# Kernel tuning notes

Measured on AMD Instinct MI355X. Metric: run time of the kernel, lower is better.

## Reference

```python
import jax, jax.numpy as jnp
import numpy as np

TOP_K = 4
N_GROUP = 4
TOPK_GROUP = 2
ROUTED_SCALING = 1.0


def setup_inputs() -> dict:
    key = jax.random.key(0)
    k1, k2, k3, k4, k5 = jax.random.split(key, 5)
    B, S, H, I, E = 1, 2048, 1024, 512, 16
    hidden_states = jax.random.normal(k1, (B, S, H), dtype=jnp.float32)
    # router weight (kaiming-uniform-like scale)
    gate_weight = jax.random.normal(k2, (E, H), dtype=jnp.float32) * (1.0 / np.sqrt(H))
    e_bias = jnp.zeros((E,), dtype=jnp.float32)  # e_score_correction_bias buffer
    gate_proj = jax.random.normal(k3, (E, I, H), dtype=jnp.float32) * 0.02
    up_proj = jax.random.normal(k4, (E, I, H), dtype=jnp.float32) * 0.02
    down_proj = jax.random.normal(k5, (E, H, I), dtype=jnp.float32) * 0.02
    return {
        "hidden_states": hidden_states,
        "gate_weight": gate_weight,
        "e_bias": e_bias,
        "gate_proj": gate_proj,
        "up_proj": up_proj,
        "down_proj": down_proj,
    }


def _route(x_flat, gate_weight, e_bias):
    # x_flat: [T, H]
    T = x_flat.shape[0]
    E = gate_weight.shape[0]
    logits = jnp.einsum("th,eh->te", x_flat, gate_weight)
    scores = jax.nn.sigmoid(logits)                      # [T, E]
    scores_for_choice = scores + e_bias[None, :]
    # group scores = sum of top-2 expert scores within each group
    grp = scores_for_choice.reshape(T, N_GROUP, E // N_GROUP)
    top2, _ = jax.lax.top_k(grp, 2)
    group_scores = top2.sum(axis=-1)                     # [T, G]
    _, group_idx = jax.lax.top_k(group_scores, TOPK_GROUP)
    group_mask = jax.nn.one_hot(group_idx, N_GROUP, dtype=scores.dtype).sum(axis=1)  # [T, G]
    score_mask = jnp.repeat(group_mask, E // N_GROUP, axis=1)                        # [T, E]
    tmp_scores = jnp.where(score_mask > 0, scores_for_choice, 0.0)
    _, topk_idx = jax.lax.top_k(tmp_scores, TOP_K)       # [T, K]
    topk_weight = jnp.take_along_axis(scores, topk_idx, axis=1)
    denom = topk_weight.sum(axis=-1, keepdims=True) + 1e-20
    topk_weight = topk_weight / denom * ROUTED_SCALING
    return topk_idx, topk_weight


def reference(hidden_states, gate_weight, e_bias, gate_proj, up_proj, down_proj):
    B, S, H = hidden_states.shape
    E = gate_proj.shape[0]
    x = hidden_states.reshape(-1, H).astype(jnp.float32)  # [T, H]
    topk_idx, topk_weight = _route(x, gate_weight, e_bias)
    # combine weights per (token, expert): sum over the k slots selecting e
    combine = (jax.nn.one_hot(topk_idx, E, dtype=x.dtype) * topk_weight[..., None]).sum(axis=1)  # [T, E]
    # dense expert MLP (mathematically equal to gather-compute-scatter since
    # non-selected experts receive zero combine weight)
    g = jnp.einsum("th,eih->tei", x, gate_proj)
    u = jnp.einsum("th,eih->tei", x, up_proj)
    act = jax.nn.silu(g) * u                              # [T, E, I]
    expert_out = jnp.einsum("tei,ehi->teh", act, down_proj)
    y = jnp.einsum("teh,te->th", expert_out, combine)
    return y.reshape(B, S, H)
```

## Files before the change

kernel.cpp:

```cpp
#include <hip/hip_runtime.h>
#include <hip/hip_bf16.h>

typedef __attribute__((ext_vector_type(8))) short bf16x8;
typedef __attribute__((ext_vector_type(4))) float f32x4;

#define T_TOK 2048
#define HD 1024
#define ID 512
#define NE 16
#define TOPK 4
#define BK 32
#define WELEM (HD*ID*NE)
#define CPAD 16

__device__ __forceinline__ unsigned pk2(float a, float b) {
    return __builtin_amdgcn_perm(__float_as_uint(b), __float_as_uint(a),
                                 0x07060302u);
}
__device__ __forceinline__ bf16x8 cvt8(const float* __restrict__ p) {
    float4 a = *(const float4*)p;
    float4 b = *(const float4*)(p + 4);
    union { bf16x8 v; unsigned u[4]; } r;
    r.u[0] = pk2(a.x, a.y); r.u[1] = pk2(a.z, a.w);
    r.u[2] = pk2(b.x, b.y); r.u[3] = pk2(b.z, b.w);
    return r.v;
}
__device__ __forceinline__ short f2bf(float f) {
    unsigned u = __float_as_uint(f);
    return (short)((u + 0x7fffu + ((u >> 16) & 1u)) >> 16);
}
__device__ __forceinline__ float bf2f(short s) {
    return __uint_as_float(((unsigned)(unsigned short)s) << 16);
}
__device__ __forceinline__ void load_lds16(const short* g, short* l) {
    __builtin_amdgcn_global_load_lds(
        (const __attribute__((address_space(1))) unsigned*)g,
        (__attribute__((address_space(3))) unsigned*)l, 16, 0, 0);
}

#define MFMA_BF16 __builtin_amdgcn_mfma_f32_16x16x32_bf16

__global__ __launch_bounds__(256) void conv_k(
        const float* __restrict__ s0, short* __restrict__ d0,
        const float* __restrict__ s1, short* __restrict__ d1,
        const float* __restrict__ s2, short* __restrict__ d2,
        int* __restrict__ counts) {
    if (blockIdx.x == 0 && blockIdx.y == 0)
        counts[threadIdx.x] = 0;
    const float* src = (blockIdx.y == 0) ? s0 : (blockIdx.y == 1) ? s1 : s2;
    short* dst       = (blockIdx.y == 0) ? d0 : (blockIdx.y == 1) ? d1 : d2;
    size_t i = ((size_t)blockIdx.x * 256 + threadIdx.x) * 8;
    union { bf16x8 v; uint4 q; } r;
    r.v = cvt8(src + i);
    *(uint4*)(dst + i) = r.q;
}

__global__ __launch_bounds__(256) void router_k(
        const float* __restrict__ x, const float* __restrict__ gw,
        const float* __restrict__ eb,
        int* __restrict__ tk_idx, float* __restrict__ tk_w,
        short* __restrict__ xb) {
    int wid  = (blockIdx.x * 256 + threadIdx.x) >> 6;
    int lane = threadIdx.x & 63;

    const float* xr = x + (size_t)wid * HD + lane * 16;
    float xv[16];
#pragma unroll
    for (int c = 0; c < 4; c++) {
        float4 v = *(const float4*)(xr + c * 4);
        xv[4 * c] = v.x; xv[4 * c + 1] = v.y; xv[4 * c + 2] = v.z; xv[4 * c + 3] = v.w;
    }
    {
        union { uint4 q; unsigned u[4]; } w0, w1;
        w0.u[0] = pk2(xv[0], xv[1]);  w0.u[1] = pk2(xv[2], xv[3]);
        w0.u[2] = pk2(xv[4], xv[5]);  w0.u[3] = pk2(xv[6], xv[7]);
        w1.u[0] = pk2(xv[8], xv[9]);  w1.u[1] = pk2(xv[10], xv[11]);
        w1.u[2] = pk2(xv[12], xv[13]); w1.u[3] = pk2(xv[14], xv[15]);
        short* d = xb + ((size_t)wid << 10) + lane * 16;
        *(uint4*)d = w0.q;
        *(uint4*)(d + 8) = w1.q;
    }

    float logits[NE];
#pragma unroll
    for (int e = 0; e < NE; e++) {
        const float* gr = gw + e * HD + lane * 16;
        float p = 0.f;
#pragma unroll
        for (int c = 0; c < 4; c++) {
            float4 v = *(const float4*)(gr + c * 4);
            p += xv[4 * c] * v.x + xv[4 * c + 1] * v.y +
                 xv[4 * c + 2] * v.z + xv[4 * c + 3] * v.w;
        }
#pragma unroll
        for (int s = 32; s > 0; s >>= 1) p += __shfl_xor(p, s, 64);
        logits[e] = p;
    }

    float scores[NE], sc[NE];
#pragma unroll
    for (int e = 0; e < NE; e++) {
        scores[e] = 1.f / (1.f + __expf(-logits[e]));
        sc[e] = scores[e] + eb[e];
    }

    float gs[4];
#pragma unroll
    for (int g = 0; g < 4; g++) {
        float a = sc[4 * g], b = sc[4 * g + 1], c = sc[4 * g + 2], d = sc[4 * g + 3];
        float h1 = fmaxf(a, b), l1 = fminf(a, b);
        float h2 = fmaxf(c, d), l2 = fminf(c, d);
        gs[g] = fmaxf(h1, h2) + fmaxf(fminf(h1, h2), fmaxf(l1, l2));
    }
    int g0 = 0; float b0 = gs[0];
#pragma unroll
    for (int g = 1; g < 4; g++) if (gs[g] > b0) { b0 = gs[g]; g0 = g; }
    int g1 = -1; float b1 = -1e30f;
#pragma unroll
    for (int g = 0; g < 4; g++) if (g != g0 && gs[g] > b1) { b1 = gs[g]; g1 = g; }

    int taken = 0;
    int bid[TOPK]; float bsc[TOPK]; float wsum = 0.f;
#pragma unroll
    for (int k = 0; k < TOPK; k++) {
        float bv = -1e30f; int bi = 0; float bs = 0.f;
#pragma unroll
        for (int e = 0; e < NE; e++) {
            int grp = e >> 2;
            bool ok = ((grp == g0) || (grp == g1)) && !((taken >> e) & 1);
            if (ok && sc[e] > bv) { bv = sc[e]; bi = e; bs = scores[e]; }
        }
        taken |= (1 << bi);
        bid[k] = bi; bsc[k] = bs; wsum += bs;
    }
    if (lane == 0) {
        float inv = 1.0f / (wsum + 1e-20f);
#pragma unroll
        for (int k = 0; k < TOPK; k++) {
            tk_idx[wid * TOPK + k] = bid[k];
            tk_w[wid * TOPK + k]   = bsc[k] * inv;
        }
    }
}

__global__ __launch_bounds__(256) void assign_k(
        const int* __restrict__ tk_idx,
        int* __restrict__ counts, int* __restrict__ tok_list,
        int* __restrict__ pair_slot) {
    int p = blockIdx.x * 256 + threadIdx.x;
    int e = tk_idx[p];
    int slot = atomicAdd(&counts[e * CPAD], 1);
    tok_list[e * T_TOK + slot] = p >> 2;
    pair_slot[p] = slot;
}

__global__ __launch_bounds__(256) void gemm1_k(
        const short* __restrict__ xb,
        const short* __restrict__ gpb,
        const short* __restrict__ upb,
        const int* __restrict__ counts,
        const int* __restrict__ tok_list,
        short* __restrict__ act) {
    __shared__ short xs[2][128 * BK];
    __shared__ short gs[2][64 * BK];
    __shared__ short us[2][64 * BK];
    __shared__ int   tok_s[128];

    int e = blockIdx.x;
    int cnt = counts[e * CPAD];
    int base = blockIdx.z * 128;
    if (base >= cnt) return;
    int off = 0;
#pragma unroll
    for (int q = 0; q < NE; q++) if (q < e) off += counts[q * CPAD];
    int arow0 = off + base;

    int tid = threadIdx.x;
    if (tid < 128) {
        int s = base + tid;
        tok_s[tid] = (s < cnt) ? tok_list[e * T_TOK + s] : tok_list[e * T_TOK];
    }
    __syncthreads();

    int wv = tid >> 6, lane = tid & 63;
    int qd = lane >> 4, l16 = lane & 15;
    int wm = (wv >> 1) * 64, wn = (wv & 1) * 32;
    int nb0 = blockIdx.y * 64;
    const short* gp = gpb + (size_t)e * ID * HD + (size_t)nb0 * HD;
    const short* up = upb + (size_t)e * ID * HD + (size_t)nb0 * HD;

    const short* xsg[2]; short* xld[2];
#pragma unroll
    for (int i = 0; i < 2; i++) {
        int idx = i * 256 + tid, r = idx >> 2, c = idx & 3;
        int f = (r >> 1) & 3;
        xsg[i] = xb + ((size_t)tok_s[r] << 10) + ((c ^ f) << 3);
        xld[i] = &xs[0][(i * 256 + wv * 64) * 8];
    }
    const short* gsg; const short* usg; short* gld; short* uld;
    {
        int r = tid >> 2, c = tid & 3;
        int f = (r >> 1) & 3;
        size_t so = (size_t)r * HD + ((c ^ f) << 3);
        gsg = gp + so;
        usg = up + so;
        gld = &gs[0][(wv * 64) * 8];
        uld = &us[0][(wv * 64) * 8];
    }

    f32x4 accg[4][2] = {};
    f32x4 accu[4][2] = {};

    auto STAGE = [&](int kp, int b) {
        load_lds16(xsg[0] + kp, xld[0] + b * (128 * BK));
        load_lds16(xsg[1] + kp, xld[1] + b * (128 * BK));
        load_lds16(gsg + kp, gld + b * (64 * BK));
        load_lds16(usg + kp, uld + b * (64 * BK));
    };
    auto COMPUTE = [&](int b) {
        const short* xsb = xs[b];
        const short* gsb = gs[b];
        const short* usb = us[b];
        bf16x8 af[4], bg[2], bu[2];
#pragma unroll
        for (int i = 0; i < 4; i++) {
            int r = wm + i * 16 + l16;
            af[i] = *(const bf16x8*)&xsb[r * BK + ((qd ^ ((r >> 1) & 3)) << 3)];
        }
#pragma unroll
        for (int j = 0; j < 2; j++) {
            int r = wn + j * 16 + l16;
            int lo = r * BK + ((qd ^ ((r >> 1) & 3)) << 3);
            bg[j] = *(const bf16x8*)&gsb[lo];
            bu[j] = *(const bf16x8*)&usb[lo];
        }
#pragma unroll
        for (int i = 0; i < 4; i++)
#pragma unroll
            for (int j = 0; j < 2; j++) {
                accg[i][j] = MFMA_BF16(af[i], bg[j], accg[i][j], 0, 0, 0);
                accu[i][j] = MFMA_BF16(af[i], bu[j], accu[i][j], 0, 0, 0);
            }
    };

    constexpr int NP = HD / BK;
    STAGE(0, 0);
    auto STEP = [&](int p, int b) {
        if (p + 1 < NP) {
            STAGE((p + 1) * BK, b ^ 1);
            asm volatile("s_waitcnt vmcnt(4)" ::: "memory");
        } else {
            asm volatile("s_waitcnt vmcnt(0)" ::: "memory");
        }
        __builtin_amdgcn_s_barrier();
        asm volatile("" ::: "memory");
        COMPUTE(b);
        asm volatile("" ::: "memory");
        __builtin_amdgcn_s_barrier();
    };
#pragma unroll 1
    for (int p = 0; p < NP; p += 2) { STEP(p, 0); STEP(p + 1, 1); }

#pragma unroll
    for (int i = 0; i < 4; i++)
#pragma unroll
        for (int j = 0; j < 2; j++)
#pragma unroll
            for (int r = 0; r < 4; r++) {
                int m = wm + i * 16 + qd * 4 + r;
                if (base + m < cnt) {
                    float g = accg[i][j][r], u = accu[i][j][r];
                    float a = g / (1.f + __expf(-g)) * u;
                    act[(size_t)(arow0 + m) * ID + nb0 + wn + j * 16 + l16] = f2bf(a);
                }
            }
}

__global__ __launch_bounds__(256) void gemm2_k(
        const short* __restrict__ act,
        const short* __restrict__ dpb,
        const int* __restrict__ counts,
        short* __restrict__ yexp) {
    __shared__ short as_[2][128 * BK];
    __shared__ short ds_[2][128 * BK];

    int e = blockIdx.x;
    int cnt = counts[e * CPAD];
    int base = blockIdx.z * 128;
    if (base >= cnt) return;
    int off = 0;
#pragma unroll
    for (int q = 0; q < NE; q++) if (q < e) off += counts[q * CPAD];
    int arow0 = off + base;

    int tid = threadIdx.x;
    int wv = tid >> 6, lane = tid & 63;
    int qd = lane >> 4, l16 = lane & 15;
    int wm = (wv >> 1) * 64, wn = (wv & 1) * 64;
    int hb0 = blockIdx.y * 128;
    const short* dp = dpb + (size_t)e * HD * ID + (size_t)hb0 * ID;

    const short* asg[2]; const short* dsg[2]; short* ald[2]; short* dld[2];
#pragma unroll
    for (int i = 0; i < 2; i++) {
        int idx = i * 256 + tid, r = idx >> 2, c = idx & 3;
        int f = (r >> 1) & 3;
        int sw = (c ^ f) << 3;
        asg[i] = act + (size_t)(arow0 + r) * ID + sw;
        dsg[i] = dp + (size_t)r * ID + sw;
        ald[i] = &as_[0][(i * 256 + wv * 64) * 8];
        dld[i] = &ds_[0][(i * 256 + wv * 64) * 8];
    }

    f32x4 acc[4][4] = {};

    auto STAGE = [&](int kp, int b) {
        load_lds16(asg[0] + kp, ald[0] + b * (128 * BK));
        load_lds16(asg[1] + kp, ald[1] + b * (128 * BK));
        load_lds16(dsg[0] + kp, dld[0] + b * (128 * BK));
        load_lds16(dsg[1] + kp, dld[1] + b * (128 * BK));
    };
    auto COMPUTE = [&](int b) {
        const short* asb = as_[b];
        const short* dsb = ds_[b];
        bf16x8 af[4], bd[4];
#pragma unroll
        for (int i = 0; i < 4; i++) {
            int r = wm + i * 16 + l16;
            af[i] = *(const bf16x8*)&asb[r * BK + ((qd ^ ((r >> 1) & 3)) << 3)];
            int r2 = wn + i * 16 + l16;
            bd[i] = *(const bf16x8*)&dsb[r2 * BK + ((qd ^ ((r2 >> 1) & 3)) << 3)];
        }
#pragma unroll
        for (int i = 0; i < 4; i++)
#pragma unroll
            for (int j = 0; j < 4; j++)
                acc[i][j] = MFMA_BF16(af[i], bd[j], acc[i][j], 0, 0, 0);
    };

    constexpr int NP = ID / BK;
    STAGE(0, 0);
    auto STEP = [&](int p, int b) {
        if (p + 1 < NP) {
            STAGE((p + 1) * BK, b ^ 1);
            asm volatile("s_waitcnt vmcnt(4)" ::: "memory");
        } else {
            asm volatile("s_waitcnt vmcnt(0)" ::: "memory");
        }
        __builtin_amdgcn_s_barrier();
        asm volatile("" ::: "memory");
        COMPUTE(b);
        asm volatile("" ::: "memory");
        __builtin_amdgcn_s_barrier();
    };
#pragma unroll 1
    for (int p = 0; p < NP; p += 2) { STEP(p, 0); STEP(p + 1, 1); }

#pragma unroll
    for (int i = 0; i < 4; i++)
#pragma unroll
        for (int j = 0; j < 4; j++)
#pragma unroll
            for (int r = 0; r < 4; r++) {
                int m = wm + i * 16 + qd * 4 + r;
                if (base + m < cnt)
                    yexp[(size_t)(arow0 + m) * HD + hb0 + wn + j * 16 + l16] =
                        f2bf(acc[i][j][r]);
            }
}

__global__ __launch_bounds__(256) void combine_k(
        const short* __restrict__ yexp,
        const int* __restrict__ counts,
        const int* __restrict__ tk_idx, const float* __restrict__ tk_w,
        const int* __restrict__ pair_slot,
        float* __restrict__ out) {
    __shared__ int offs_s[NE];
    if (threadIdx.x == 0) {
        int a = 0;
#pragma unroll
        for (int e = 0; e < NE; e++) { offs_s[e] = a; a += counts[e * CPAD]; }
    }
    __syncthreads();

    int t = blockIdx.x * 2 + (threadIdx.x >> 7);
    int i = threadIdx.x & 127;
    float acc[8] = {};
#pragma unroll
    for (int k = 0; k < TOPK; k++) {
        int p = t * TOPK + k;
        int e = tk_idx[p];
        int row = offs_s[e] + pair_slot[p];
        float w = tk_w[p];
        bf16x8 v = *(const bf16x8*)(yexp + (size_t)row * HD + i * 8);
#pragma unroll
        for (int j = 0; j < 8; j++) acc[j] += w * bf2f(v[j]);
    }
    float4 o0 = {acc[0], acc[1], acc[2], acc[3]};
    float4 o1 = {acc[4], acc[5], acc[6], acc[7]};
    float* d = out + (size_t)t * HD + i * 8;
    *(float4*)d = o0;
    *(float4*)(d + 4) = o1;
}

extern "C" void kernel_launch(void* const* d_in, const int* in_sizes, int n_in,
                              void* d_out, int out_size, void* d_ws, size_t ws_size,
                              hipStream_t stream) {
    const float* x  = (const float*)d_in[0];
    const float* gw = (const float*)d_in[1];
    const float* eb = (const float*)d_in[2];
    const float* gp = (const float*)d_in[3];
    const float* up = (const float*)d_in[4];
    const float* dp = (const float*)d_in[5];

    short* gpb = (short*)d_ws;
    short* upb = gpb + WELEM;
    short* dpb = upb + WELEM;
    short* xb  = dpb + WELEM;
    short* act = xb + (size_t)T_TOK * HD;
    int* counts    = (int*)(act + (size_t)(T_TOK * TOPK + 128) * ID);
    int* tok_list  = counts + NE * CPAD;
    int* pair_slot = tok_list + NE * T_TOK;
    int* tk_idx    = pair_slot + T_TOK * TOPK;
    float* tk_w    = (float*)(tk_idx + T_TOK * TOPK);
    short* yexp = gpb;

    conv_k<<<dim3(WELEM / 8 / 256, 3), 256, 0, stream>>>(gp, gpb, up, upb,
                                                         dp, dpb, counts);
    router_k<<<T_TOK / 4, 256, 0, stream>>>(x, gw, eb, tk_idx, tk_w, xb);
    assign_k<<<T_TOK * TOPK / 256, 256, 0, stream>>>(tk_idx, counts,
                                                     tok_list, pair_slot);
    gemm1_k<<<dim3(NE, ID / 64, T_TOK / 128), 256, 0, stream>>>(
        xb, gpb, upb, counts, tok_list, act);
    gemm2_k<<<dim3(NE, HD / 128, T_TOK / 128), 256, 0, stream>>>(
        act, dpb, counts, yexp);
    combine_k<<<T_TOK / 2, 256, 0, stream>>>(yexp, counts, tk_idx, tk_w,
                                             pair_slot, (float*)d_out);
}
```

Measured before the change: 222.4 us.

## Triple-buffer GEMM shared-memory pipelines and fold expert assignment into router

Both expert GEMM kernels move from double-buffered to triple-buffered LDS staging, prefetching two K-tiles ahead with adjusted vmcnt waits so global loads have more time to land before compute. Separately, the token-to-expert slot assignment (atomic counts, token list, pair slots) is folded into the router kernel, which removes one kernel launch. The extra buffer raises LDS use per block and may lower occupancy. The in-router atomics now run inside the routing kernel rather than in their own launch.

```diff
diff --git a/kernel.cpp b/kernel.cpp
--- a/kernel.cpp
+++ b/kernel.cpp
@@ -59,7 +59,9 @@
         const float* __restrict__ x, const float* __restrict__ gw,
         const float* __restrict__ eb,
         int* __restrict__ tk_idx, float* __restrict__ tk_w,
-        short* __restrict__ xb) {
+        short* __restrict__ xb,
+        int* __restrict__ counts, int* __restrict__ tok_list,
+        int* __restrict__ pair_slot) {
     int wid  = (blockIdx.x * 256 + threadIdx.x) >> 6;
     int lane = threadIdx.x & 63;
 
@@ -133,25 +135,15 @@
         taken |= (1 << bi);
         bid[k] = bi; bsc[k] = bs; wsum += bs;
     }
-    if (lane == 0) {
+    if (lane < TOPK) {
         float inv = 1.0f / (wsum + 1e-20f);
-#pragma unroll
-        for (int k = 0; k < TOPK; k++) {
-            tk_idx[wid * TOPK + k] = bid[k];
-            tk_w[wid * TOPK + k]   = bsc[k] * inv;
-        }
-    }
-}
-
-__global__ __launch_bounds__(256) void assign_k(
-        const int* __restrict__ tk_idx,
-        int* __restrict__ counts, int* __restrict__ tok_list,
-        int* __restrict__ pair_slot) {
-    int p = blockIdx.x * 256 + threadIdx.x;
-    int e = tk_idx[p];
-    int slot = atomicAdd(&counts[e * CPAD], 1);
-    tok_list[e * T_TOK + slot] = p >> 2;
-    pair_slot[p] = slot;
+        int ee = bid[lane];
+        int slot = atomicAdd(&counts[ee * CPAD], 1);
+        tok_list[ee * T_TOK + slot] = wid;
+        pair_slot[wid * TOPK + lane] = slot;
+        tk_idx[wid * TOPK + lane] = ee;
+        tk_w[wid * TOPK + lane]   = bsc[lane] * inv;
+    }
 }
 
 __global__ __launch_bounds__(256) void gemm1_k(
@@ -161,9 +153,9 @@
         const int* __restrict__ counts,
         const int* __restrict__ tok_list,
         short* __restrict__ act) {
-    __shared__ short xs[2][128 * BK];
-    __shared__ short gs[2][64 * BK];
-    __shared__ short us[2][64 * BK];
+    __shared__ short xs[3][128 * BK];
+    __shared__ short gs[3][64 * BK];
+    __shared__ short us[3][64 * BK];
     __shared__ int   tok_s[128];
 
     int e = blockIdx.x;
@@ -244,10 +236,15 @@
     };
 
     constexpr int NP = HD / BK;
-    STAGE(0, 0);
-    auto STEP = [&](int p, int b) {
-        if (p + 1 < NP) {
-            STAGE((p + 1) * BK, b ^ 1);
+    STAGE(0, 0); STAGE(BK, 1);
+    int b = 0;
+#pragma unroll 1
+    for (int p = 0; p < NP; ++p) {
+        int bn = b + 2; if (bn >= 3) bn -= 3;
+        if (p + 2 < NP) {
+            STAGE((p + 2) * BK, bn);
+            asm volatile("s_waitcnt vmcnt(8)" ::: "memory");
+        } else if (p + 1 < NP) {
             asm volatile("s_waitcnt vmcnt(4)" ::: "memory");
         } else {
             asm volatile("s_waitcnt vmcnt(0)" ::: "memory");
@@ -257,9 +254,8 @@
         COMPUTE(b);
         asm volatile("" ::: "memory");
         __builtin_amdgcn_s_barrier();
-    };
-#pragma unroll 1
-    for (int p = 0; p < NP; p += 2) { STEP(p, 0); STEP(p + 1, 1); }
+        b = (b == 2) ? 0 : b + 1;
+    }
 
 #pragma unroll
     for (int i = 0; i < 4; i++)
@@ -281,8 +277,8 @@
         const short* __restrict__ dpb,
         const int* __restrict__ counts,
         short* __restrict__ yexp) {
-    __shared__ short as_[2][128 * BK];
-    __shared__ short ds_[2][128 * BK];
+    __shared__ short as_[3][128 * BK];
+    __shared__ short ds_[3][128 * BK];
 
     int e = blockIdx.x;
     int cnt = counts[e * CPAD];
@@ -339,10 +335,15 @@
     };
 
     constexpr int NP = ID / BK;
-    STAGE(0, 0);
-    auto STEP = [&](int p, int b) {
-        if (p + 1 < NP) {
-            STAGE((p + 1) * BK, b ^ 1);
+    STAGE(0, 0); STAGE(BK, 1);
+    int b = 0;
+#pragma unroll 1
+    for (int p = 0; p < NP; ++p) {
+        int bn = b + 2; if (bn >= 3) bn -= 3;
+        if (p + 2 < NP) {
+            STAGE((p + 2) * BK, bn);
+            asm volatile("s_waitcnt vmcnt(8)" ::: "memory");
+        } else if (p + 1 < NP) {
             asm volatile("s_waitcnt vmcnt(4)" ::: "memory");
         } else {
             asm volatile("s_waitcnt vmcnt(0)" ::: "memory");
@@ -352,9 +353,8 @@
         COMPUTE(b);
         asm volatile("" ::: "memory");
         __builtin_amdgcn_s_barrier();
-    };
-#pragma unroll 1
-    for (int p = 0; p < NP; p += 2) { STEP(p, 0); STEP(p + 1, 1); }
+        b = (b == 2) ? 0 : b + 1;
+    }
 
 #pragma unroll
     for (int i = 0; i < 4; i++)
@@ -427,9 +427,8 @@
 
     conv_k<<<dim3(WELEM / 8 / 256, 3), 256, 0, stream>>>(gp, gpb, up, upb,
                                                          dp, dpb, counts);
-    router_k<<<T_TOK / 4, 256, 0, stream>>>(x, gw, eb, tk_idx, tk_w, xb);
-    assign_k<<<T_TOK * TOPK / 256, 256, 0, stream>>>(tk_idx, counts,
-                                                     tok_list, pair_slot);
+    router_k<<<T_TOK / 4, 256, 0, stream>>>(x, gw, eb, tk_idx, tk_w, xb,
+                                            counts, tok_list, pair_slot);
     gemm1_k<<<dim3(NE, ID / 64, T_TOK / 128), 256, 0, stream>>>(
         xb, gpb, upb, counts, tok_list, act);
     gemm2_k<<<dim3(NE, HD / 128, T_TOK / 128), 256, 0, stream>>>(
```

Result: faster. 214.3 us (-3.6%).
